# Kernel tuning notes

Measured on AMD Instinct MI355X. Metric: run time of the kernel, lower is better.

## Reference

```python
import jax, jax.numpy as jnp
import numpy as np

N_NODES = 100000
N_EDGES = 1600000
D_IN = 128
D_H = 128
NUM_GRAPHS = 128


def setup_inputs() -> dict:
    key = jax.random.key(0)
    ks = jax.random.split(key, 16)
    x = jax.random.normal(ks[0], (N_NODES, D_IN), dtype=jnp.float32)
    edge_index = jax.random.randint(ks[1], (2, N_EDGES), 0, N_NODES, dtype=jnp.int64)
    batch_index = jnp.sort(jax.random.randint(ks[2], (N_NODES,), 0, NUM_GRAPHS, dtype=jnp.int64))
    s = 0.05
    W1 = s * jax.random.normal(ks[3], (D_IN, D_H), dtype=jnp.float32)
    b1 = jnp.zeros((D_H,), jnp.float32)
    W2 = s * jax.random.normal(ks[4], (D_H, D_H), dtype=jnp.float32)
    b2 = jnp.zeros((D_H,), jnp.float32)
    W3 = s * jax.random.normal(ks[5], (D_H, D_H), dtype=jnp.float32)
    b3 = jnp.zeros((D_H,), jnp.float32)
    W4 = s * jax.random.normal(ks[6], (D_H, D_H), dtype=jnp.float32)
    b4 = jnp.zeros((D_H,), jnp.float32)
    Wl = s * jax.random.normal(ks[7], (2 * D_H, 1), dtype=jnp.float32)
    bl = jnp.zeros((1,), jnp.float32)
    return {"x": x, "edge_index": edge_index, "batch_index": batch_index,
            "W1": W1, "b1": b1, "W2": W2, "b2": b2, "W3": W3, "b3": b3,
            "W4": W4, "b4": b4, "Wl": Wl, "bl": bl}


def _gcn_prep(edge_index, n_nodes):
    # add self-loops, symmetric normalization D^-1/2 (A+I) D^-1/2
    loops = jnp.arange(n_nodes, dtype=edge_index.dtype)
    row = jnp.concatenate([edge_index[0], loops])  # source
    col = jnp.concatenate([edge_index[1], loops])  # target
    deg = jax.ops.segment_sum(jnp.ones_like(col, dtype=jnp.float32), col,
                              num_segments=n_nodes)
    dinv = jnp.where(deg > 0, jax.lax.rsqrt(jnp.maximum(deg, 1.0)), 0.0)
    norm = dinv[row] * dinv[col]  # [E+N]
    return row, col, norm


def _gcn(h, W, b, row, col, norm, n_nodes):
    h = h @ W                                   # [N, H]
    msg = h[row] * norm[:, None]                # gather + scale
    return jax.ops.segment_sum(msg, col, num_segments=n_nodes) + b


def reference(x, edge_index, batch_index, W1, b1, W2, b2, W3, b3, W4, b4, Wl, bl):
    n = x.shape[0]
    row, col, norm = _gcn_prep(edge_index, n)
    h = jnp.tanh(_gcn(x, W1, b1, row, col, norm, n))
    h = jnp.tanh(_gcn(h, W2, b2, row, col, norm, n))
    h = jnp.tanh(_gcn(h, W3, b3, row, col, norm, n))
    h = jnp.tanh(_gcn(h, W4, b4, row, col, norm, n))
    # global max / mean pool per graph
    cnt = jax.ops.segment_sum(jnp.ones((n,), jnp.float32), batch_index,
                              num_segments=NUM_GRAPHS)
    mx = jax.ops.segment_max(h, batch_index, num_segments=NUM_GRAPHS)
    mx = jnp.where(cnt[:, None] > 0, mx, 0.0)
    sm = jax.ops.segment_sum(h, batch_index, num_segments=NUM_GRAPHS)
    mn = sm / jnp.maximum(cnt, 1.0)[:, None]
    pooled = jnp.concatenate([mx, mn], axis=1)  # [G, 2H]
    return pooled @ Wl + bl                     # [G, 1]
```

## Files before the change

### kernel.cpp

```cpp
#include <hip/hip_runtime.h>
#include <hip/hip_bf16.h>
#include <math.h>

#define PSPLIT 8
#define BSH 8
#define NBMAX 512
#define CHUNK 8192
#define AST 40

typedef float v4f __attribute__((ext_vector_type(4)));
typedef float v2f __attribute__((ext_vector_type(2)));
typedef unsigned int v4u __attribute__((ext_vector_type(4)));
typedef unsigned int v2u __attribute__((ext_vector_type(2)));
typedef __attribute__((ext_vector_type(8))) short bf8;
typedef __attribute__((ext_vector_type(4))) float f4;
typedef unsigned short u16;
typedef unsigned int u32;

static inline size_t align_up(size_t x, size_t a){ return (x + a - 1) & ~(a - 1); }

__device__ inline void bf_split(float v, u16& hi, u16& lo){
  __hip_bfloat16 h = __float2bfloat16(v);
  float hf = __bfloat162float(h);
  __hip_bfloat16 l = __float2bfloat16(v - hf);
  hi = *(u16*)&h; lo = *(u16*)&l;
}

__device__ inline void fmixlo(float& a, u32 p){
  asm("v_fma_mix_f32 %0, %1, 1.0, %0 op_sel:[0,0,0] op_sel_hi:[1,0,0]" : "+v"(a) : "v"(p));
}
__device__ inline void fmixhi(float& a, u32 p){
  asm("v_fma_mix_f32 %0, %1, 1.0, %0 op_sel:[1,0,0] op_sel_hi:[1,0,0]" : "+v"(a) : "v"(p));
}

__device__ inline float f16lo(u32 p){ u16 q = (u16)p; return (float)*(_Float16*)&q; }
__device__ inline float f16hi(u32 p){ u16 q = (u16)(p >> 16); return (float)*(_Float16*)&q; }

__device__ inline float tanh_fast(float x){
  float u = __builtin_amdgcn_exp2f(x * 2.8853900817779268f);
  float q = __builtin_amdgcn_rcpf(u + 1.0f);
  return fmaf(-2.0f, q, 1.0f);
}


__global__ __launch_bounds__(256) void k_bhist(const int* __restrict__ col, int* __restrict__ bcnt,
                                               int E, int NB,
                                               const int* __restrict__ batch, int* __restrict__ gstart,
                                               int n, int G){
  extern __shared__ int lh[];
  for (int i = threadIdx.x; i < NB; i += 256) lh[i] = 0;
  __syncthreads();
  for (int e = blockIdx.x * 256 + threadIdx.x; e < E; e += gridDim.x * 256)
    atomicAdd(&lh[col[e] >> BSH], 1);
  __syncthreads();
  for (int i = threadIdx.x; i < NB; i += 256){
    int v = lh[i];
    if (v) atomicAdd(&bcnt[i], v);
  }
  for (int i = blockIdx.x * 256 + threadIdx.x; i < n; i += gridDim.x * 256){
    int cb = batch[i];
    if (i == 0){ for (int g = 0; g <= cb; ++g) gstart[g] = 0; }
    else { int pb = batch[i - 1]; for (int g = pb + 1; g <= cb; ++g) gstart[g] = i; }
    if (i == n - 1){ for (int g = cb + 1; g <= G; ++g) gstart[g] = n; }
  }
}

__global__ void k_bscan(const int* __restrict__ bcnt, int* __restrict__ boff, int NB, int E,
                        int* __restrict__ rp, int N){
  __shared__ int sd[256];
  int t = threadIdx.x;
  int c[16]; int s = 0;
  const int PT = (NB + 255) / 256;
  for (int j = 0; j < PT; ++j){ int i = t * PT + j; c[j] = (i < NB) ? bcnt[i] : 0; s += c[j]; }
  sd[t] = s; __syncthreads();
  for (int off = 1; off < 256; off <<= 1){
    int v = sd[t];
    if (t >= off) v += sd[t - off];
    __syncthreads(); sd[t] = v; __syncthreads();
  }
  int run = sd[t] - s;
  for (int j = 0; j < PT; ++j){ int i = t * PT + j; if (i < NB) boff[i] = run; run += c[j]; }
  if (t == 255){ boff[NB] = run; rp[N] = E; }
}

__global__ __launch_bounds__(256) void k_bscat(const int* __restrict__ ei, const int* __restrict__ boff,
                                               int* __restrict__ bfill, unsigned* __restrict__ tmp,
                                               int E, int NB){
  __shared__ int lh[NBMAX], loff[NBMAX], gb[NBMAX], lfil[NBMAX];
  __shared__ int sd[256];
  __shared__ int sumA;
  __shared__ u32 stg[CHUNK];
  int t = threadIdx.x;
  const int* col = ei + E;
  int c0 = blockIdx.x * CHUNK;
  int c1 = c0 + CHUNK; if (c1 > E) c1 = E;

  for (int i = t; i < NBMAX; i += 256){ lh[i] = 0; lfil[i] = 0; }
  __syncthreads();
  for (int e = c0 + t; e < c1; e += 256)
    atomicAdd(&lh[col[e] >> BSH], 1);
  __syncthreads();
  sd[t] = lh[t]; __syncthreads();
  for (int off = 1; off < 256; off <<= 1){
    int v = sd[t];
    if (t >= off) v += sd[t - off];
    __syncthreads(); sd[t] = v; __syncthreads();
  }
  loff[t] = sd[t] - lh[t];
  if (t == 255) sumA = sd[255];
  __syncthreads();
  int lb = lh[256 + t];
  sd[t] = lb; __syncthreads();
  for (int off = 1; off < 256; off <<= 1){
    int v = sd[t];
    if (t >= off) v += sd[t - off];
    __syncthreads(); sd[t] = v; __syncthreads();
  }
  loff[256 + t] = sumA + sd[t] - lb;
  for (int i = t; i < NB; i += 256){
    int c = lh[i];
    gb[i] = c ? (boff[i] + atomicAdd(&bfill[i * 16], c)) : 0;
  }
  __syncthreads();
  for (int e = c0 + t; e < c1; e += 256){
    int d = col[e], s = ei[e];
    int b = d >> BSH;
    int p = atomicAdd(&lfil[b], 1);
    stg[loff[b] + p] = (unsigned)s | ((unsigned)(d & 255) << 17);
  }
  __syncthreads();
  int wv = t >> 6, lane = t & 63;
  for (int b = wv; b < NB; b += 4){
    int len = lh[b];
    if (!len) continue;
    int base = gb[b], lo = loff[b];
    for (int j = lane; j < len; j += 64) tmp[base + j] = stg[lo + j];
  }
}

__global__ __launch_bounds__(256) void k_bfin(const unsigned* __restrict__ tmp, const int* __restrict__ boff,
                                              int* __restrict__ ssrc, int* __restrict__ rp,
                                              float* __restrict__ dinv, int N){
  int b = blockIdx.x;
  int d0 = b << BSH;
  int lim = N - d0; if (lim > 256) lim = 256;
  __shared__ int dcnt[256], dexc[256], lfill[256];
  int t = threadIdx.x;
  dcnt[t] = 0; lfill[t] = 0;
  __syncthreads();
  int lo = boff[b], hi = boff[b + 1];
  for (int i = lo + t; i < hi; i += 256) atomicAdd(&dcnt[tmp[i] >> 17], 1);
  __syncthreads();
  int cme = dcnt[t];
  dexc[t] = cme; __syncthreads();
  for (int off = 1; off < 256; off <<= 1){
    int v = dexc[t];
    if (t >= off) v += dexc[t - off];
    __syncthreads(); dexc[t] = v; __syncthreads();
  }
  int excl = dexc[t] - cme;
  __syncthreads();
  dexc[t] = excl;
  if (t < lim){
    int d = d0 + t;
    rp[d] = lo + excl;
    double dd = (double)(cme + 1);
    dinv[d] = (float)(1.0 / sqrt(dd));
  }
  __syncthreads();
  for (int i = lo + t; i < hi; i += 256){
    unsigned r = tmp[i];
    int l = r >> 17;
    int pos = dexc[l] + atomicAdd(&lfill[l], 1);
    ssrc[lo + pos] = (int)(r & 0x1FFFFu);
  }
}


__global__ __launch_bounds__(256) void k_cvtw(const float* __restrict__ w0, const float* __restrict__ w1,
                                              const float* __restrict__ w2, const float* __restrict__ w3,
                                              u16* __restrict__ wth, u16* __restrict__ wtl){
  int id = blockIdx.x * 256 + threadIdx.x;
  if (id >= 4 * 16384) return;
  int l = id >> 14, rem = id & 16383, k = rem >> 7, nn = rem & 127;
  const float* Wsrc = (l == 0) ? w0 : (l == 1) ? w1 : (l == 2) ? w2 : w3;
  float v = Wsrc[k * 128 + nn];
  u16 hi, lo; bf_split(v, hi, lo);
  wth[(l << 14) + nn * 128 + k] = hi;
  wtl[(l << 14) + nn * 128 + k] = lo;
}


__global__ __launch_bounds__(256, 4) void k_gemm(const float* __restrict__ A,
                                                 const u16* __restrict__ wth, const u16* __restrict__ wtl,
                                                 const float* __restrict__ dinv,
                                                 u16* __restrict__ C, int n, int packed){
  __shared__ u16 Ah[128 * AST], Al[128 * AST], Wh[128 * AST], Wl[128 * AST];
  int t = threadIdx.x;
  int r0 = blockIdx.x * 128;
  int wv = t >> 6, lane = t & 63;
  int q = lane >> 4, ln = lane & 15;

  int srow = t >> 1;
  int shalf = (t & 1) * 16;
  int grow = r0 + srow; if (grow > n - 1) grow = n - 1;
  const float* ga = A + (size_t)grow * 128 + shalf;
  const u32* gap = (const u32*)A + (size_t)grow * 64 + (shalf >> 1);
  const u16* gwh = wth + srow * 128 + shalf;
  const u16* gwl = wtl + srow * 128 + shalf;

  f4 acc[2][8];
  #pragma unroll
  for (int mt = 0; mt < 2; ++mt)
    #pragma unroll
    for (int nt = 0; nt < 8; ++nt) acc[mt][nt] = (f4)(0.f);

  for (int c = 0; c < 4; ++c){
    __syncthreads();
    {
      u16* ah = &Ah[srow * AST + shalf];
      u16* al = &Al[srow * AST + shalf];
      if (packed){
        const v4u* gp = (const v4u*)(gap + c * 16);
        v4u vv0 = gp[0], vv1 = gp[1];
        u32 w_[8] = {vv0.x, vv0.y, vv0.z, vv0.w, vv1.x, vv1.y, vv1.z, vv1.w};
        #pragma unroll
        for (int i = 0; i < 4; ++i){
          u32 wa = w_[i * 2], wb = w_[i * 2 + 1];
          float x0 = f16lo(wa), x1 = f16hi(wa), x2 = f16lo(wb), x3 = f16hi(wb);
          u16 h0,h1,h2,h3,l0,l1,l2,l3;
          bf_split(x0, h0, l0); bf_split(x1, h1, l1);
          bf_split(x2, h2, l2); bf_split(x3, h3, l3);
          ushort4 hv = {h0,h1,h2,h3}, lv = {l0,l1,l2,l3};
          *(ushort4*)&ah[i * 4] = hv;
          *(ushort4*)&al[i * 4] = lv;
        }
      } else {
        const float4* gp = (const float4*)(ga + c * 32);
        #pragma unroll
        for (int i = 0; i < 4; ++i){
          float4 v = gp[i];
          u16 h0,h1,h2,h3,l0,l1,l2,l3;
          bf_split(v.x, h0, l0); bf_split(v.y, h1, l1);
          bf_split(v.z, h2, l2); bf_split(v.w, h3, l3);
          ushort4 hv = {h0,h1,h2,h3}, lv = {l0,l1,l2,l3};
          *(ushort4*)&ah[i * 4] = hv;
          *(ushort4*)&al[i * 4] = lv;
        }
      }
    }
    {
      const u16* ph = gwh + c * 32;
      const u16* pl = gwl + c * 32;
      bf8 h0 = *(const bf8*)ph, h1 = *(const bf8*)(ph + 8);
      bf8 l0 = *(const bf8*)pl, l1 = *(const bf8*)(pl + 8);
      *(bf8*)&Wh[srow * AST + shalf] = h0; *(bf8*)&Wh[srow * AST + shalf + 8] = h1;
      *(bf8*)&Wl[srow * AST + shalf] = l0; *(bf8*)&Wl[srow * AST + shalf + 8] = l1;
    }
    __syncthreads();

    bf8 afh[2], afl[2];
    #pragma unroll
    for (int mt = 0; mt < 2; ++mt){
      int row = wv * 32 + mt * 16 + ln;
      afh[mt] = *(const bf8*)&Ah[row * AST + q * 8];
      afl[mt] = *(const bf8*)&Al[row * AST + q * 8];
    }
    #pragma unroll
    for (int nt = 0; nt < 8; ++nt){
      int wn = nt * 16 + ln;
      bf8 wfh = *(const bf8*)&Wh[wn * AST + q * 8];
      bf8 wfl = *(const bf8*)&Wl[wn * AST + q * 8];
      #pragma unroll
      for (int mt = 0; mt < 2; ++mt){
        acc[mt][nt] = __builtin_amdgcn_mfma_f32_16x16x32_bf16(afh[mt], wfh, acc[mt][nt], 0, 0, 0);
        acc[mt][nt] = __builtin_amdgcn_mfma_f32_16x16x32_bf16(afl[mt], wfh, acc[mt][nt], 0, 0, 0);
        acc[mt][nt] = __builtin_amdgcn_mfma_f32_16x16x32_bf16(afh[mt], wfl, acc[mt][nt], 0, 0, 0);
      }
    }
  }

  #pragma unroll
  for (int mt = 0; mt < 2; ++mt){
    int base_m = r0 + wv * 32 + mt * 16 + q * 4;
    float dv[4];
    #pragma unroll
    for (int reg = 0; reg < 4; ++reg){
      int row = base_m + reg;
      dv[reg] = (row < n) ? dinv[row] : 0.f;
    }
    #pragma unroll
    for (int nt = 0; nt < 8; ++nt){
      #pragma unroll
      for (int reg = 0; reg < 4; ++reg){
        int row = base_m + reg;
        if (row < n){
          _Float16 hv = (_Float16)(acc[mt][nt][reg] * dv[reg]);
          C[(size_t)row * 128 + nt * 16 + ln] = *(u16*)&hv;
        }
      }
    }
  }
}


__global__ __launch_bounds__(256) void k_agg(const u16* __restrict__ hwp, const int* __restrict__ rp,
                                             const int* __restrict__ ssrc,
                                             const float* __restrict__ dinv, const float* __restrict__ bias,
                                             u32* __restrict__ hout, int n){
  int node = blockIdx.x * 4 + (threadIdx.x >> 6);
  node = __builtin_amdgcn_readfirstlane(node);
  if (node >= n) return;
  int lane = threadIdx.x & 63;
  const u32* hw32 = (const u32*)hwp;

  int e0 = rp[node], e1 = rp[node + 1];
  float a0 = 0.f, a1 = 0.f;
  int e = e0;
  while (e + 16 <= e1){
    u32 p[16];
    #pragma unroll
    for (int i = 0; i < 16; ++i){
      int s = ssrc[e + i];
      p[i] = hw32[(size_t)s * 64 + lane];
    }
    #pragma unroll
    for (int i = 0; i < 16; ++i){ fmixlo(a0, p[i]); fmixhi(a1, p[i]); }
    e += 16;
  }
  while (e + 4 <= e1){
    u32 p[4];
    #pragma unroll
    for (int i = 0; i < 4; ++i){
      int s = ssrc[e + i];
      p[i] = hw32[(size_t)s * 64 + lane];
    }
    #pragma unroll
    for (int i = 0; i < 4; ++i){ fmixlo(a0, p[i]); fmixhi(a1, p[i]); }
    e += 4;
  }
  while (e < e1){
    int s = ssrc[e];
    u32 p = hw32[(size_t)s * 64 + lane];
    fmixlo(a0, p); fmixhi(a1, p);
    ++e;
  }
  {
    u32 p = hw32[(size_t)node * 64 + lane];
    fmixlo(a0, p); fmixhi(a1, p);
  }
  float di = dinv[node];
  v2f bv = *(const v2f*)(bias + lane * 2);
  float r0 = tanh_fast(fmaf(a0, di, bv.x));
  float r1 = tanh_fast(fmaf(a1, di, bv.y));
  _Float16 f0 = (_Float16)r0, f1 = (_Float16)r1;
  u32 pv = ((u32)(*(u16*)&f1) << 16) | (u32)(*(u16*)&f0);
  __builtin_nontemporal_store(pv, hout + (size_t)node * 64 + lane);
}


__global__ __launch_bounds__(256) void k_pool1(const u32* __restrict__ h, const int* __restrict__ gstart,
                                               float* __restrict__ pmx, float* __restrict__ psm){
  int g = blockIdx.x >> 3, s = blockIdx.x & (PSPLIT - 1);
  int t = threadIdx.x;
  int fq = t & 31;
  int rw = t >> 5;
  int i0 = gstart[g], i1 = gstart[g + 1];
  int len = i1 - i0;
  int chunk = (len + PSPLIT - 1) / PSPLIT;
  int a = i0 + s * chunk;
  int b = a + chunk; if (b > i1) b = i1;

  const v2u* hv = (const v2u*)h;
  v4f mx = (v4f)(-INFINITY), sm = (v4f)(0.f);
  for (int i = a + rw; i < b; i += 8){
    v2u p = hv[(size_t)i * 32 + fq];
    float x0 = f16lo(p.x), x1 = f16hi(p.x), x2 = f16lo(p.y), x3 = f16hi(p.y);
    mx.x = fmaxf(mx.x, x0); mx.y = fmaxf(mx.y, x1);
    mx.z = fmaxf(mx.z, x2); mx.w = fmaxf(mx.w, x3);
    sm.x += x0; sm.y += x1; sm.z += x2; sm.w += x3;
  }
  __shared__ v4f smx[8][32], ssm[8][32];
  smx[rw][fq] = mx; ssm[rw][fq] = sm;
  __syncthreads();
  if (rw == 0){
    #pragma unroll
    for (int r2 = 1; r2 < 8; ++r2){
      v4f m2 = smx[r2][fq], s2 = ssm[r2][fq];
      mx.x = fmaxf(mx.x, m2.x); mx.y = fmaxf(mx.y, m2.y);
      mx.z = fmaxf(mx.z, m2.z); mx.w = fmaxf(mx.w, m2.w);
      sm += s2;
    }
    ((v4f*)pmx)[(size_t)blockIdx.x * 32 + fq] = mx;
    ((v4f*)psm)[(size_t)blockIdx.x * 32 + fq] = sm;
  }
}

__global__ __launch_bounds__(128) void k_head(const float* __restrict__ pmx, const float* __restrict__ psm,
                                              const int* __restrict__ gstart,
                                              const float* __restrict__ Wl, const float* __restrict__ bl,
                                              float* __restrict__ out){
  int g = blockIdx.x, f = threadIdx.x;
  float mx = -INFINITY, sm = 0.f;
  #pragma unroll
  for (int s = 0; s < PSPLIT; ++s){
    mx = fmaxf(mx, pmx[((size_t)g * PSPLIT + s) * 128 + f]);
    sm += psm[((size_t)g * PSPLIT + s) * 128 + f];
  }
  int cnt = gstart[g + 1] - gstart[g];
  if (cnt <= 0) mx = 0.f;
  float mn = sm / (float)(cnt > 0 ? cnt : 1);
  float contrib = mx * Wl[f] + mn * Wl[128 + f];
  for (int o = 32; o > 0; o >>= 1) contrib += __shfl_down(contrib, o);
  __shared__ float sred[2];
  if ((f & 63) == 0) sred[f >> 6] = contrib;
  __syncthreads();
  if (f == 0) out[g] = sred[0] + sred[1] + bl[0];
}


extern "C" void kernel_launch(void* const* d_in, const int* in_sizes, int n_in,
                              void* d_out, int out_size, void* d_ws, size_t ws_size,
                              hipStream_t stream){
  const float* x     = (const float*)d_in[0];
  const int*   ei    = (const int*)d_in[1];
  const int*   batch = (const int*)d_in[2];
  const float* W[4]  = {(const float*)d_in[3], (const float*)d_in[5], (const float*)d_in[7], (const float*)d_in[9]};
  const float* B[4]  = {(const float*)d_in[4], (const float*)d_in[6], (const float*)d_in[8], (const float*)d_in[10]};
  const float* Wl    = (const float*)d_in[11];
  const float* bl    = (const float*)d_in[12];
  float* out = (float*)d_out;

  int N = in_sizes[0] / 128;
  int E = in_sizes[1] / 2;
  int G = out_size;
  int NB = (N + 255) >> BSH;

  char* ws = (char*)d_ws;
  size_t off = 0;
  auto alloc = [&](size_t bytes) -> void* {
    void* p = ws + off; off = align_up(off + bytes, 256); return p;
  };
  float* dinv  = (float*)alloc((size_t)N * 4);
  int*   rp    = (int*)  alloc((size_t)(N + 1) * 4);
  int*   bcnt  = (int*)  alloc((size_t)(NB + 1) * 4);
  int*   boff  = (int*)  alloc((size_t)(NB + 1) * 4);
  int*   bfill = (int*)  alloc((size_t)NB * 16 * 4);
  int*   gst   = (int*)  alloc((size_t)(G + 1) * 4);
  int*   ssrc  = (int*)  alloc((size_t)E * 4);
  u16*   wth   = (u16*)  alloc((size_t)4 * 16384 * 2);
  u16*   wtl   = (u16*)  alloc((size_t)4 * 16384 * 2);
  float* pmx   = (float*)alloc((size_t)G * PSPLIT * 128 * 4);
  float* psm   = (float*)alloc((size_t)G * PSPLIT * 128 * 4);
  u16*   hw    = (u16*)  alloc((size_t)N * 128 * 2);
  u32*   h     = (u32*)  alloc((size_t)N * 64 * 4);
  unsigned* tmp = (unsigned*)hw;

  hipMemsetAsync(bcnt, 0, (size_t)(NB + 1) * 4, stream);
  hipMemsetAsync(bfill, 0, (size_t)NB * 16 * 4, stream);

  k_cvtw <<<256, 256, 0, stream>>>(W[0], W[1], W[2], W[3], wth, wtl);
  k_bhist<<<128, 256, NB * 4, stream>>>(ei + E, bcnt, E, NB, batch, gst, N, G);
  k_bscan<<<1, 256, 0, stream>>>(bcnt, boff, NB, E, rp, N);
  k_bscat<<<(E + CHUNK - 1) / CHUNK, 256, 0, stream>>>(ei, boff, bfill, tmp, E, NB);
  k_bfin <<<NB, 256, 0, stream>>>(tmp, boff, ssrc, rp, dinv, N);

  int gemmG = (N + 127) / 128;
  int aggG  = (N + 3) / 4;
  const float* hin = x;
  for (int l = 0; l < 4; ++l){
    k_gemm<<<gemmG, 256, 0, stream>>>(hin, wth + (l << 14), wtl + (l << 14), dinv, hw, N, l > 0);
    k_agg <<<aggG, 256, 0, stream>>>(hw, rp, ssrc, dinv, B[l], h, N);
    hin = (const float*)h;
  }
  k_pool1<<<G * PSPLIT, 256, 0, stream>>>(h, gst, pmx, psm);
  k_head <<<G, 128, 0, stream>>>(pmx, psm, gst, Wl, bl, out);
}
```

Before: 535.1 us.

## Slice node features into 8 feature-major blocks and split aggregation per slice

Stores the fp16 node feature matrix as eight 16-feature slices, each contiguous across nodes (32 bytes per node per slice), instead of row-major 256-byte rows. The aggregation kernel now launches one block group per slice, so each wave handles 8 edges at once with 8 lanes per edge, followed by a cross-lane reduction. GEMM loads/stores and pooling are adapted to the sliced layout. The aim is a smaller per-slice working set for the random gather, improving cache hit rates. The cost is 8x more aggregation blocks, repeated index reads per slice and 32-byte gather segments.

```diff
diff --git a/kernel.cpp b/kernel.cpp
--- a/kernel.cpp
+++ b/kernel.cpp
@@ -205,7 +205,6 @@
   int shalf = (t & 1) * 16;
   int grow = r0 + srow; if (grow > n - 1) grow = n - 1;
   const float* ga = A + (size_t)grow * 128 + shalf;
-  const u32* gap = (const u32*)A + (size_t)grow * 64 + (shalf >> 1);
   const u16* gwh = wth + srow * 128 + shalf;
   const u16* gwl = wtl + srow * 128 + shalf;
 
@@ -221,8 +220,9 @@
       u16* ah = &Ah[srow * AST + shalf];
       u16* al = &Al[srow * AST + shalf];
       if (packed){
-        const v4u* gp = (const v4u*)(gap + c * 16);
-        v4u vv0 = gp[0], vv1 = gp[1];
+        const u32* gp32 = (const u32*)A + ((size_t)(2 * c + (shalf >> 4)) * n + grow) * 8;
+        v4u vv0 = *(const v4u*)gp32;
+        v4u vv1 = *(const v4u*)(gp32 + 4);
         u32 w_[8] = {vv0.x, vv0.y, vv0.z, vv0.w, vv1.x, vv1.y, vv1.z, vv1.w};
         #pragma unroll
         for (int i = 0; i < 4; ++i){
@@ -291,12 +291,13 @@
     }
     #pragma unroll
     for (int nt = 0; nt < 8; ++nt){
+      u16* Cs = C + (size_t)nt * n * 16;
       #pragma unroll
       for (int reg = 0; reg < 4; ++reg){
         int row = base_m + reg;
         if (row < n){
           _Float16 hv = (_Float16)(acc[mt][nt][reg] * dv[reg]);
-          C[(size_t)row * 128 + nt * 16 + ln] = *(u16*)&hv;
+          Cs[(size_t)row * 16 + ln] = *(u16*)&hv;
         }
       }
     }
@@ -308,59 +309,70 @@
                                              const int* __restrict__ ssrc,
                                              const float* __restrict__ dinv, const float* __restrict__ bias,
                                              u32* __restrict__ hout, int n){
-  int node = blockIdx.x * 4 + (threadIdx.x >> 6);
+  int slice = blockIdx.x & 7;
+  int node = (blockIdx.x >> 3) * 4 + (threadIdx.x >> 6);
   node = __builtin_amdgcn_readfirstlane(node);
   if (node >= n) return;
   int lane = threadIdx.x & 63;
-  const u32* hw32 = (const u32*)hwp;
+  int el = lane >> 3;
+  int fl = lane & 7;
+  size_t sstr = (size_t)n * 8;
+  const u32* base = (const u32*)hwp + (size_t)slice * sstr + fl;
 
   int e0 = rp[node], e1 = rp[node + 1];
   float a0 = 0.f, a1 = 0.f;
-  int e = e0;
-  while (e + 16 <= e1){
-    u32 p[16];
-    #pragma unroll
-    for (int i = 0; i < 16; ++i){
-      int s = ssrc[e + i];
-      p[i] = hw32[(size_t)s * 64 + lane];
-    }
-    #pragma unroll
-    for (int i = 0; i < 16; ++i){ fmixlo(a0, p[i]); fmixhi(a1, p[i]); }
-    e += 16;
-  }
-  while (e + 4 <= e1){
-    u32 p[4];
-    #pragma unroll
-    for (int i = 0; i < 4; ++i){
-      int s = ssrc[e + i];
-      p[i] = hw32[(size_t)s * 64 + lane];
-    }
-    #pragma unroll
-    for (int i = 0; i < 4; ++i){ fmixlo(a0, p[i]); fmixhi(a1, p[i]); }
-    e += 4;
-  }
-  while (e < e1){
-    int s = ssrc[e];
-    u32 p = hw32[(size_t)s * 64 + lane];
+  for (int eb = e0; eb < e1; eb += 64){
+    int m = e1 - eb; if (m > 64) m = 64;
+    int sl = (lane < m) ? ssrc[eb + lane] : 0;
+    int mp = m & ~7;
+    int j = 0;
+    for (; j + 32 <= mp; j += 32){
+      int s0 = __shfl(sl, j + el),      s1 = __shfl(sl, j + 8 + el);
+      int s2 = __shfl(sl, j + 16 + el), s3 = __shfl(sl, j + 24 + el);
+      u32 p0 = base[(size_t)s0 * 8], p1 = base[(size_t)s1 * 8];
+      u32 p2 = base[(size_t)s2 * 8], p3 = base[(size_t)s3 * 8];
+      fmixlo(a0, p0); fmixhi(a1, p0); fmixlo(a0, p1); fmixhi(a1, p1);
+      fmixlo(a0, p2); fmixhi(a1, p2); fmixlo(a0, p3); fmixhi(a1, p3);
+    }
+    if (j + 16 <= mp){
+      int s0 = __shfl(sl, j + el), s1 = __shfl(sl, j + 8 + el);
+      u32 p0 = base[(size_t)s0 * 8], p1 = base[(size_t)s1 * 8];
+      fmixlo(a0, p0); fmixhi(a1, p0); fmixlo(a0, p1); fmixhi(a1, p1);
+      j += 16;
+    }
+    if (j + 8 <= mp){
+      int s0 = __shfl(sl, j + el);
+      u32 p0 = base[(size_t)s0 * 8];
+      fmixlo(a0, p0); fmixhi(a1, p0);
+      j += 8;
+    }
+    if (j < m){
+      int s0 = __shfl(sl, j + el);
+      if (j + el < m){
+        u32 p0 = base[(size_t)s0 * 8];
+        fmixlo(a0, p0); fmixhi(a1, p0);
+      }
+    }
+  }
+  a0 += __shfl_down(a0, 32); a1 += __shfl_down(a1, 32);
+  a0 += __shfl_down(a0, 16); a1 += __shfl_down(a1, 16);
+  a0 += __shfl_down(a0, 8);  a1 += __shfl_down(a1, 8);
+  if (lane < 8){
+    u32 p = base[(size_t)node * 8];
     fmixlo(a0, p); fmixhi(a1, p);
-    ++e;
-  }
-  {
-    u32 p = hw32[(size_t)node * 64 + lane];
-    fmixlo(a0, p); fmixhi(a1, p);
-  }
-  float di = dinv[node];
-  v2f bv = *(const v2f*)(bias + lane * 2);
-  float r0 = tanh_fast(fmaf(a0, di, bv.x));
-  float r1 = tanh_fast(fmaf(a1, di, bv.y));
-  _Float16 f0 = (_Float16)r0, f1 = (_Float16)r1;
-  u32 pv = ((u32)(*(u16*)&f1) << 16) | (u32)(*(u16*)&f0);
-  __builtin_nontemporal_store(pv, hout + (size_t)node * 64 + lane);
+    float di = dinv[node];
+    v2f bv = *(const v2f*)(bias + slice * 16 + fl * 2);
+    float r0 = tanh_fast(fmaf(a0, di, bv.x));
+    float r1 = tanh_fast(fmaf(a1, di, bv.y));
+    _Float16 f0 = (_Float16)r0, f1 = (_Float16)r1;
+    u32 pv = ((u32)(*(u16*)&f1) << 16) | (u32)(*(u16*)&f0);
+    __builtin_nontemporal_store(pv, hout + (size_t)slice * sstr + (size_t)node * 8 + fl);
+  }
 }
 
 
 __global__ __launch_bounds__(256) void k_pool1(const u32* __restrict__ h, const int* __restrict__ gstart,
-                                               float* __restrict__ pmx, float* __restrict__ psm){
+                                               float* __restrict__ pmx, float* __restrict__ psm, int n){
   int g = blockIdx.x >> 3, s = blockIdx.x & (PSPLIT - 1);
   int t = threadIdx.x;
   int fq = t & 31;
@@ -371,10 +383,10 @@
   int a = i0 + s * chunk;
   int b = a + chunk; if (b > i1) b = i1;
 
-  const v2u* hv = (const v2u*)h;
+  const u32* sb = h + (size_t)(fq >> 2) * n * 8 + (fq & 3) * 2;
   v4f mx = (v4f)(-INFINITY), sm = (v4f)(0.f);
   for (int i = a + rw; i < b; i += 8){
-    v2u p = hv[(size_t)i * 32 + fq];
+    v2u p = *(const v2u*)(sb + (size_t)i * 8);
     float x0 = f16lo(p.x), x1 = f16hi(p.x), x2 = f16lo(p.y), x3 = f16hi(p.y);
     mx.x = fmaxf(mx.x, x0); mx.y = fmaxf(mx.y, x1);
     mx.z = fmaxf(mx.z, x2); mx.w = fmaxf(mx.w, x3);
@@ -466,13 +478,13 @@
   k_bfin <<<NB, 256, 0, stream>>>(tmp, boff, ssrc, rp, dinv, N);
 
   int gemmG = (N + 127) / 128;
-  int aggG  = (N + 3) / 4;
+  int aggG  = 8 * ((N + 3) / 4);
   const float* hin = x;
   for (int l = 0; l < 4; ++l){
     k_gemm<<<gemmG, 256, 0, stream>>>(hin, wth + (l << 14), wtl + (l << 14), dinv, hw, N, l > 0);
     k_agg <<<aggG, 256, 0, stream>>>(hw, rp, ssrc, dinv, B[l], h, N);
     hin = (const float*)h;
   }
-  k_pool1<<<G * PSPLIT, 256, 0, stream>>>(h, gst, pmx, psm);
+  k_pool1<<<G * PSPLIT, 256, 0, stream>>>(h, gst, pmx, psm, N);
   k_head <<<G, 128, 0, stream>>>(pmx, psm, gst, Wl, bl, out);
 }
```

After: 1.019 ms. +90.4%, slower.
